# Kernel optimization log

Measured on AMD Instinct MI355X. Metric: run time of the kernel, lower is better.

Reference implementation:

```python
import math
import jax, jax.numpy as jnp
import numpy as np

B, N, DIN, DOUT = 64, 512, 256, 256
EPS = 1e-5  # torch BatchNorm1d default


def setup_inputs() -> dict:
    key = jax.random.key(0)
    k0, k1, k2, k3 = jax.random.split(key, 4)
    x = jax.random.normal(k0, (B, N, DIN), dtype=jnp.float32)
    # row-scaled dense adjacency (keeps activation magnitudes sane)
    adj = jax.random.uniform(k1, (B, N, N), dtype=jnp.float32) / N
    # prefix-style masks: first L_i nodes of each graph are valid
    lengths = jax.random.randint(k2, (B,), N // 4, N + 1)
    mask = (jnp.arange(N)[None, :] < lengths[:, None]).astype(jnp.float32)
    # xavier_normal_ init for weight
    std = math.sqrt(2.0 / (DIN + DOUT))
    weight = jax.random.normal(k3, (DIN, DOUT), dtype=jnp.float32) * std
    bias = jnp.zeros((DOUT,), dtype=jnp.float32)
    gamma = jnp.ones((DOUT,), dtype=jnp.float32)   # BN affine scale
    beta = jnp.zeros((DOUT,), dtype=jnp.float32)   # BN affine shift
    return {"x": x, "adj": adj, "mask": mask, "weight": weight,
            "bias": bias, "gamma": gamma, "beta": beta}


def reference(x, adj, mask, weight, bias, gamma, beta):
    # y = adj @ x @ W + b
    y = jnp.einsum('bnm,bmd->bnd', adj, x)
    y = jnp.einsum('bnd,de->bne', y, weight) + bias
    # masked BatchNorm1d (training mode): batch stats over all valid nodes,
    # equivalent to the torch code's pack -> BN -> unpack on prefix masks.
    m = mask[:, :, None]                       # [B, N, 1]
    n = jnp.sum(mask)                          # total valid nodes
    mean = jnp.sum(y * m, axis=(0, 1)) / n     # [DOUT]
    var = jnp.sum(((y - mean) ** 2) * m, axis=(0, 1)) / n  # biased var
    y = ((y - mean) * jax.lax.rsqrt(var + EPS) * gamma + beta) * m
    return jax.nn.relu(y)
```

## Files before the change

kernel.cpp:

```cpp
#include <hip/hip_runtime.h>

#define B_    64
#define N_    512
#define DIN_  256
#define DOUT_ 256
#define EPS_  1e-5f
#define ROWS_ (B_ * N_)
#define NBLK_Y2 512

typedef __attribute__((ext_vector_type(8))) short bf16x8;
typedef __attribute__((ext_vector_type(8))) unsigned short u16x8;
typedef __attribute__((ext_vector_type(4))) float f32x4;
typedef __attribute__((ext_vector_type(4))) short short4v;

__device__ __forceinline__ short f2bf(float f) {
    unsigned u = __builtin_bit_cast(unsigned, f);
    u += 0x7fff + ((u >> 16) & 1);
    return (short)(u >> 16);
}


__global__ __launch_bounds__(256) void wt_cvt(const float* __restrict__ W,
                                              short* __restrict__ WTf) {
    const int c = blockIdx.x * 256 + threadIdx.x;
    const int kf = c >> 10, ef = (c >> 6) & 15, lp = c & 63;
    const int e = ef * 16 + (lp & 15);
    const int k0 = kf * 32 + (lp >> 4) * 8;
    bf16x8 h;
    #pragma unroll
    for (int j = 0; j < 8; ++j)
        h[j] = f2bf(W[(size_t)(k0 + j) * DOUT_ + e]);
    *(bf16x8*)&WTf[(size_t)c * 8] = h;
}

__global__ __launch_bounds__(512, 4) void gemm_xw(const float* __restrict__ X,
                                                  const short* __restrict__ WTf,
                                                  short* __restrict__ xwT) {
    __shared__ __align__(16) short As[8 * 4 * 64 * 8];
    const int tid = threadIdx.x, wv = tid >> 6, lane = tid & 63;
    const int lrow = lane & 15, lg = lane >> 4;
    const int bid = blockIdx.x;
    const int rt = ((bid & 7) * 8 + ((bid >> 3) & 7)) * 8 + (bid >> 6);
    const int rowBase = rt * 64;

    #pragma unroll
    for (int j = 0; j < 4; ++j) {
        int s = tid + j * 512;
        int kf = s >> 8, mf = (s >> 6) & 3, lp = s & 63;
        int row = mf * 16 + (lp & 15);
        int k = kf * 32 + (lp >> 4) * 8;
        const float* src = &X[(size_t)(rowBase + row) * DIN_ + k];
        float4 v0 = *(const float4*)src;
        float4 v1 = *(const float4*)(src + 4);
        bf16x8 h = { f2bf(v0.x), f2bf(v0.y), f2bf(v0.z), f2bf(v0.w),
                     f2bf(v1.x), f2bf(v1.y), f2bf(v1.z), f2bf(v1.w) };
        *(bf16x8*)&As[s * 8] = h;
    }
    __syncthreads();

    const short* b0p = WTf + ((size_t)(wv * 2 + 0) * 64 + lane) * 8;
    const short* b1p = WTf + ((size_t)(wv * 2 + 1) * 64 + lane) * 8;
    bf16x8 bc0 = *(const bf16x8*)(b0p);
    bf16x8 bc1 = *(const bf16x8*)(b1p);
    f32x4 acc[4][2] = {};
    #pragma unroll 2
    for (int c = 0; c < 8; ++c) {
        const int cn = (c + 1 < 8) ? c + 1 : 7;
        bf16x8 bn0 = *(const bf16x8*)(b0p + cn * 8192);
        bf16x8 bn1 = *(const bf16x8*)(b1p + cn * 8192);
        const short* ab = &As[(c * 256 + lane) * 8];
        bf16x8 a0 = *(const bf16x8*)(ab);
        bf16x8 a1 = *(const bf16x8*)(ab + 512);
        bf16x8 a2 = *(const bf16x8*)(ab + 1024);
        bf16x8 a3 = *(const bf16x8*)(ab + 1536);
        acc[0][0] = __builtin_amdgcn_mfma_f32_16x16x32_bf16(a0, bc0, acc[0][0], 0, 0, 0);
        acc[0][1] = __builtin_amdgcn_mfma_f32_16x16x32_bf16(a0, bc1, acc[0][1], 0, 0, 0);
        acc[1][0] = __builtin_amdgcn_mfma_f32_16x16x32_bf16(a1, bc0, acc[1][0], 0, 0, 0);
        acc[1][1] = __builtin_amdgcn_mfma_f32_16x16x32_bf16(a1, bc1, acc[1][1], 0, 0, 0);
        acc[2][0] = __builtin_amdgcn_mfma_f32_16x16x32_bf16(a2, bc0, acc[2][0], 0, 0, 0);
        acc[2][1] = __builtin_amdgcn_mfma_f32_16x16x32_bf16(a2, bc1, acc[2][1], 0, 0, 0);
        acc[3][0] = __builtin_amdgcn_mfma_f32_16x16x32_bf16(a3, bc0, acc[3][0], 0, 0, 0);
        acc[3][1] = __builtin_amdgcn_mfma_f32_16x16x32_bf16(a3, bc1, acc[3][1], 0, 0, 0);
        bc0 = bn0; bc1 = bn1;
    }

    const int bz = rt >> 3, kfbase = (rt & 7) * 2;
    short* xwb = xwT + (size_t)bz * 131072;
    #pragma unroll
    for (int m = 0; m < 4; ++m)
        #pragma unroll
        for (int nf = 0; nf < 2; ++nf) {
            int kf = kfbase + (m >> 1);
            int ef = wv * 2 + nf;
            int lanep = lrow + 16 * ((m & 1) * 2 + (lg >> 1));
            size_t off = ((size_t)(kf * 16 + ef) * 64 + lanep) * 8 + (lg & 1) * 4;
            short4v o = { f2bf(acc[m][nf][0]), f2bf(acc[m][nf][1]),
                          f2bf(acc[m][nf][2]), f2bf(acc[m][nf][3]) };
            *(short4v*)&xwb[off] = o;
        }
}

template <bool BF16Y2>
__global__ __launch_bounds__(512, 4) void gemm_y2(const float* __restrict__ adj,
                                                  const short* __restrict__ xwT,
                                                  const float* __restrict__ bias,
                                                  const float* __restrict__ mask,
                                                  float* __restrict__ outf,
                                                  unsigned short* __restrict__ y2b,
                                                  float* __restrict__ psum,
                                                  float* __restrict__ psumsq,
                                                  float* __restrict__ pcnt) {
    __shared__ __align__(16) short As[16 * 4 * 64 * 8];
    const int tid = threadIdx.x, wv = tid >> 6, lane = tid & 63;
    const int lrow = lane & 15, lg = lane >> 4;
    const int bid = blockIdx.x;
    const int swz = ((bid & 7) << 6) | (bid >> 3);
    const int bz = swz >> 3, mt = swz & 7;
    const int rowBase = mt * 64;
    const float* A = adj + (size_t)bz * N_ * N_;
    const short* xwb = xwT + (size_t)bz * 131072;

    #pragma unroll
    for (int j = 0; j < 8; ++j) {
        int s = tid + j * 512;
        int kf = s >> 8, mf = (s >> 6) & 3, lp = s & 63;
        int row = mf * 16 + (lp & 15);
        int k = kf * 32 + (lp >> 4) * 8;
        const float* src = &A[(size_t)(rowBase + row) * N_ + k];
        float4 v0 = *(const float4*)src;
        float4 v1 = *(const float4*)(src + 4);
        bf16x8 h = { f2bf(v0.x), f2bf(v0.y), f2bf(v0.z), f2bf(v0.w),
                     f2bf(v1.x), f2bf(v1.y), f2bf(v1.z), f2bf(v1.w) };
        *(bf16x8*)&As[s * 8] = h;
    }
    __syncthreads();

    const short* b0p = xwb + ((size_t)(wv * 2 + 0) * 64 + lane) * 8;
    const short* b1p = xwb + ((size_t)(wv * 2 + 1) * 64 + lane) * 8;
    bf16x8 bpre[4][2];
    #pragma unroll
    for (int p = 0; p < 3; ++p) {
        bpre[p][0] = *(const bf16x8*)(b0p + p * 8192);
        bpre[p][1] = *(const bf16x8*)(b1p + p * 8192);
    }
    f32x4 acc[4][2] = {};
    #pragma unroll
    for (int c = 0; c < 16; ++c) {
        const int cn = (c + 3 < 16) ? c + 3 : 15;
        bpre[(c + 3) & 3][0] = *(const bf16x8*)(b0p + cn * 8192);
        bpre[(c + 3) & 3][1] = *(const bf16x8*)(b1p + cn * 8192);
        const short* ab = &As[(c * 256 + lane) * 8];
        bf16x8 a0 = *(const bf16x8*)(ab);
        bf16x8 a1 = *(const bf16x8*)(ab + 512);
        bf16x8 a2 = *(const bf16x8*)(ab + 1024);
        bf16x8 a3 = *(const bf16x8*)(ab + 1536);
        bf16x8 bc0 = bpre[c & 3][0];
        bf16x8 bc1 = bpre[c & 3][1];
        acc[0][0] = __builtin_amdgcn_mfma_f32_16x16x32_bf16(a0, bc0, acc[0][0], 0, 0, 0);
        acc[0][1] = __builtin_amdgcn_mfma_f32_16x16x32_bf16(a0, bc1, acc[0][1], 0, 0, 0);
        acc[1][0] = __builtin_amdgcn_mfma_f32_16x16x32_bf16(a1, bc0, acc[1][0], 0, 0, 0);
        acc[1][1] = __builtin_amdgcn_mfma_f32_16x16x32_bf16(a1, bc1, acc[1][1], 0, 0, 0);
        acc[2][0] = __builtin_amdgcn_mfma_f32_16x16x32_bf16(a2, bc0, acc[2][0], 0, 0, 0);
        acc[2][1] = __builtin_amdgcn_mfma_f32_16x16x32_bf16(a2, bc1, acc[2][1], 0, 0, 0);
        acc[3][0] = __builtin_amdgcn_mfma_f32_16x16x32_bf16(a3, bc0, acc[3][0], 0, 0, 0);
        acc[3][1] = __builtin_amdgcn_mfma_f32_16x16x32_bf16(a3, bc1, acc[3][1], 0, 0, 0);
    }

    float* C = outf + (size_t)bz * N_ * DOUT_;
    unsigned short* Cb = y2b + (size_t)bz * N_ * DOUT_;
    float mv[4][4];
    #pragma unroll
    for (int m = 0; m < 4; ++m)
        #pragma unroll
        for (int r = 0; r < 4; ++r)
            mv[m][r] = mask[bz * N_ + rowBase + m * 16 + lg * 4 + r];
    float sv[2] = {0.f, 0.f}, sq[2] = {0.f, 0.f};
    #pragma unroll
    for (int nf = 0; nf < 2; ++nf) {
        const int col = wv * 32 + nf * 16 + lrow;
        const float bv = bias[col];
        #pragma unroll
        for (int m = 0; m < 4; ++m) {
            const int r0 = rowBase + m * 16 + lg * 4;
            #pragma unroll
            for (int r = 0; r < 4; ++r) {
                float v = acc[m][nf][r] + bv;
                if (BF16Y2)
                    Cb[(size_t)(r0 + r) * DOUT_ + col] = (unsigned short)f2bf(v);
                else
                    C[(size_t)(r0 + r) * DOUT_ + col] = v;
                float vm = v * mv[m][r];
                sv[nf] += vm;
                sq[nf] = fmaf(v, vm, sq[nf]);
            }
        }
    }
    #pragma unroll
    for (int nf = 0; nf < 2; ++nf) {
        sv[nf] += __shfl_xor(sv[nf], 16); sv[nf] += __shfl_xor(sv[nf], 32);
        sq[nf] += __shfl_xor(sq[nf], 16); sq[nf] += __shfl_xor(sq[nf], 32);
    }
    const int pidx = bz * 8 + mt;
    if (lg == 0) {
        #pragma unroll
        for (int nf = 0; nf < 2; ++nf) {
            psum[(size_t)pidx * DOUT_ + wv * 32 + nf * 16 + lrow]   = sv[nf];
            psumsq[(size_t)pidx * DOUT_ + wv * 32 + nf * 16 + lrow] = sq[nf];
        }
    }
    if (wv == 0) {
        float cnt = mask[bz * N_ + rowBase + lane];
        #pragma unroll
        for (int i = 1; i < 64; i <<= 1) cnt += __shfl_xor(cnt, i);
        if (lane == 0) pcnt[pidx] = cnt;
    }
}

__global__ __launch_bounds__(256) void finalize2(const float* __restrict__ psum,
                                                 const float* __restrict__ psumsq,
                                                 const float* __restrict__ pcnt,
                                                 const float* __restrict__ gamma,
                                                 const float* __restrict__ beta,
                                                 float* __restrict__ scsh) {
    const int e = blockIdx.x, t = threadIdx.x;
    float s  = psum[(size_t)t * DOUT_ + e]   + psum[(size_t)(t + 256) * DOUT_ + e];
    float ss = psumsq[(size_t)t * DOUT_ + e] + psumsq[(size_t)(t + 256) * DOUT_ + e];
    float n  = pcnt[t] + pcnt[t + 256];
    #pragma unroll
    for (int i = 1; i < 64; i <<= 1) {
        s += __shfl_xor(s, i); ss += __shfl_xor(ss, i); n += __shfl_xor(n, i);
    }
    __shared__ float red[3][4];
    const int wv = t >> 6;
    if ((t & 63) == 0) { red[0][wv] = s; red[1][wv] = ss; red[2][wv] = n; }
    __syncthreads();
    if (t == 0) {
        s  = red[0][0] + red[0][1] + red[0][2] + red[0][3];
        ss = red[1][0] + red[1][1] + red[1][2] + red[1][3];
        n  = red[2][0] + red[2][1] + red[2][2] + red[2][3];
        float mean = s / n;
        float var = ss / n - mean * mean;
        float sc = rsqrtf(var + EPS_) * gamma[e];
        scsh[e] = sc;
        scsh[DOUT_ + e] = beta[e] - mean * sc;
    }
}

__global__ __launch_bounds__(256) void norm_relu_bf(const unsigned short* __restrict__ y2b,
                                                    const float* __restrict__ mask,
                                                    const float* __restrict__ scsh,
                                                    float* __restrict__ out) {
    const int nq = ROWS_ * (DOUT_ / 8);
    for (int q = blockIdx.x * blockDim.x + threadIdx.x; q < nq;
         q += gridDim.x * blockDim.x) {
        int e8 = (q & 31) * 8;
        int r = q >> 5;
        float m = mask[r];
        u16x8 uv = *(const u16x8*)&y2b[(size_t)q * 8];
        float4 sc0 = *(const float4*)&scsh[e8];
        float4 sc1 = *(const float4*)&scsh[e8 + 4];
        float4 sh0 = *(const float4*)&scsh[DOUT_ + e8];
        float4 sh1 = *(const float4*)&scsh[DOUT_ + e8 + 4];
        float4 o0, o1;
        #pragma unroll
        for (int j = 0; j < 4; ++j) {
            float f = __builtin_bit_cast(float, (unsigned)uv[j] << 16);
            (&o0.x)[j] = fmaxf(fmaf(f, (&sc0.x)[j], (&sh0.x)[j]) * m, 0.f);
        }
        #pragma unroll
        for (int j = 0; j < 4; ++j) {
            float f = __builtin_bit_cast(float, (unsigned)uv[j + 4] << 16);
            (&o1.x)[j] = fmaxf(fmaf(f, (&sc1.x)[j], (&sh1.x)[j]) * m, 0.f);
        }
        *(float4*)&out[(size_t)q * 8] = o0;
        *(float4*)&out[(size_t)q * 8 + 4] = o1;
    }
}

__global__ __launch_bounds__(256) void norm_relu_f32(float* __restrict__ y2,
                                                     const float* __restrict__ mask,
                                                     const float* __restrict__ scsh) {
    const int nq = ROWS_ * (DOUT_ / 4);
    for (int q = blockIdx.x * blockDim.x + threadIdx.x; q < nq;
         q += gridDim.x * blockDim.x) {
        int e4 = (q & 63) * 4;
        int r = q >> 6;
        float m = mask[r];
        float4 v  = *(float4*)&y2[(size_t)q * 4];
        float4 sc = *(const float4*)&scsh[e4];
        float4 sh = *(const float4*)&scsh[DOUT_ + e4];
        v.x = fmaxf(fmaf(v.x, sc.x, sh.x) * m, 0.f);
        v.y = fmaxf(fmaf(v.y, sc.y, sh.y) * m, 0.f);
        v.z = fmaxf(fmaf(v.z, sc.z, sh.z) * m, 0.f);
        v.w = fmaxf(fmaf(v.w, sc.w, sh.w) * m, 0.f);
        *(float4*)&y2[(size_t)q * 4] = v;
    }
}

extern "C" void kernel_launch(void* const* d_in, const int* in_sizes, int n_in,
                              void* d_out, int out_size, void* d_ws, size_t ws_size,
                              hipStream_t stream) {
    const float* x      = (const float*)d_in[0];
    const float* adj    = (const float*)d_in[1];
    const float* mask   = (const float*)d_in[2];
    const float* weight = (const float*)d_in[3];
    const float* bias   = (const float*)d_in[4];
    const float* gamma  = (const float*)d_in[5];
    const float* beta   = (const float*)d_in[6];
    float* out = (float*)d_out;

    const size_t xw_elems = (size_t)DOUT_ * ROWS_;
    const size_t need_bf = 131072 + xw_elems * 2 * 2 +
                           (size_t)NBLK_Y2 * DOUT_ * 4 * 2 + NBLK_Y2 * 4 + 2048 + 64;
    const bool use_bf = ws_size >= need_bf;

    short* WTf    = (short*)d_ws;
    short* xwT    = WTf + 256 * 256;
    unsigned short* y2b = (unsigned short*)(xwT + xw_elems);
    float* psum   = use_bf ? (float*)(y2b + xw_elems) : (float*)(y2b);
    float* psumsq = psum + NBLK_Y2 * DOUT_;
    float* pcnt   = psumsq + NBLK_Y2 * DOUT_;
    float* scsh   = pcnt + NBLK_Y2;

    wt_cvt<<<32, 256, 0, stream>>>(weight, WTf);
    gemm_xw<<<512, 512, 0, stream>>>(x, WTf, xwT);
    if (use_bf) {
        gemm_y2<true><<<NBLK_Y2, 512, 0, stream>>>(adj, xwT, bias, mask, out, y2b,
                                                   psum, psumsq, pcnt);
        finalize2<<<256, 256, 0, stream>>>(psum, psumsq, pcnt, gamma, beta, scsh);
        norm_relu_bf<<<2048, 256, 0, stream>>>(y2b, mask, scsh, out);
    } else {
        gemm_y2<false><<<NBLK_Y2, 512, 0, stream>>>(adj, xwT, bias, mask, out, y2b,
                                                    psum, psumsq, pcnt);
        finalize2<<<256, 256, 0, stream>>>(psum, psumsq, pcnt, gamma, beta, scsh);
        norm_relu_f32<<<2048, 256, 0, stream>>>(out, mask, scsh);
    }
}
```

Measured before the change: 55.52 us.

## Pre-convert adjacency to fragment-ordered bf16 and stream it directly in GEMM

```diff
diff --git a/kernel.cpp b/kernel.cpp
--- a/kernel.cpp
+++ b/kernel.cpp
@@ -31,6 +31,42 @@
     for (int j = 0; j < 8; ++j)
         h[j] = f2bf(W[(size_t)(k0 + j) * DOUT_ + e]);
     *(bf16x8*)&WTf[(size_t)c * 8] = h;
+}
+
+__global__ __launch_bounds__(512) void adj_cvt(const float* __restrict__ adj,
+                                               short* __restrict__ adjf) {
+    __shared__ short L[32 * 520];
+    const int tid = threadIdx.x;
+    const int bid = blockIdx.x;
+    const int swz = ((bid & 7) << 6) | (bid >> 3);
+    const int bz = swz >> 3, mt = swz & 7;
+    const float* A = adj + (size_t)bz * N_ * N_ + (size_t)mt * 64 * N_;
+    short* out = adjf + (size_t)(bz * 8 + mt) * 32768;
+
+    #pragma unroll
+    for (int h = 0; h < 2; ++h) {
+        if (h) __syncthreads();
+        const float* Ah = A + (size_t)h * 32 * N_;
+        #pragma unroll
+        for (int j = 0; j < 8; ++j) {
+            int o = j * 512 + tid;
+            int row = o >> 7, c4 = o & 127;
+            float4 v = *(const float4*)&Ah[(size_t)row * N_ + c4 * 4];
+            short4v s4 = { f2bf(v.x), f2bf(v.y), f2bf(v.z), f2bf(v.w) };
+            *(short4v*)&L[row * 520 + c4 * 4] = s4;
+        }
+        __syncthreads();
+        #pragma unroll
+        for (int j = 0; j < 4; ++j) {
+            int sh = j * 512 + tid;
+            int kf = sh >> 7, mfh = (sh >> 6) & 1, lp = sh & 63;
+            int rl = mfh * 16 + (lp & 15);
+            int k  = kf * 32 + (lp >> 4) * 8;
+            bf16x8 v = *(const bf16x8*)&L[rl * 520 + k];
+            int s = kf * 256 + (h * 2 + mfh) * 64 + lp;
+            *(bf16x8*)&out[(size_t)s * 8] = v;
+        }
+    }
 }
 
 __global__ __launch_bounds__(512, 4) void gemm_xw(const float* __restrict__ X,
@@ -101,15 +137,109 @@
 }
 
 template <bool BF16Y2>
-__global__ __launch_bounds__(512, 4) void gemm_y2(const float* __restrict__ adj,
-                                                  const short* __restrict__ xwT,
-                                                  const float* __restrict__ bias,
-                                                  const float* __restrict__ mask,
-                                                  float* __restrict__ outf,
-                                                  unsigned short* __restrict__ y2b,
-                                                  float* __restrict__ psum,
-                                                  float* __restrict__ psumsq,
-                                                  float* __restrict__ pcnt) {
+__global__ __launch_bounds__(512, 2) void gemm_y2f(const short* __restrict__ adjf,
+                                                   const short* __restrict__ xwT,
+                                                   const float* __restrict__ bias,
+                                                   const float* __restrict__ mask,
+                                                   float* __restrict__ outf,
+                                                   unsigned short* __restrict__ y2b,
+                                                   float* __restrict__ psum,
+                                                   float* __restrict__ psumsq,
+                                                   float* __restrict__ pcnt) {
+    const int tid = threadIdx.x, wv = tid >> 6, lane = tid & 63;
+    const int lrow = lane & 15, lg = lane >> 4;
+    const int bid = blockIdx.x;
+    const int swz = ((bid & 7) << 6) | (bid >> 3);
+    const int bz = swz >> 3, mt = swz & 7;
+    const int rowBase = mt * 64;
+    const short* ab  = adjf + (size_t)(bz * 8 + mt) * 32768;
+    const short* xwb = xwT + (size_t)bz * 131072;
+    const short* b0p = xwb + ((size_t)(wv * 2 + 0) * 64 + lane) * 8;
+    const short* b1p = xwb + ((size_t)(wv * 2 + 1) * 64 + lane) * 8;
+
+    bf16x8 aP[2][4], bP[2][2];
+    #pragma unroll
+    for (int m = 0; m < 4; ++m)
+        aP[0][m] = *(const bf16x8*)(ab + ((size_t)(0 * 4 + m) * 64 + lane) * 8);
+    bP[0][0] = *(const bf16x8*)(b0p);
+    bP[0][1] = *(const bf16x8*)(b1p);
+
+    f32x4 acc[4][2] = {};
+    #pragma unroll
+    for (int kf = 0; kf < 16; ++kf) {
+        const int cur = kf & 1, nxt = cur ^ 1;
+        if (kf < 15) {
+            #pragma unroll
+            for (int m = 0; m < 4; ++m)
+                aP[nxt][m] = *(const bf16x8*)(ab + ((size_t)((kf + 1) * 4 + m) * 64 + lane) * 8);
+            bP[nxt][0] = *(const bf16x8*)(b0p + (kf + 1) * 8192);
+            bP[nxt][1] = *(const bf16x8*)(b1p + (kf + 1) * 8192);
+        }
+        #pragma unroll
+        for (int m = 0; m < 4; ++m) {
+            acc[m][0] = __builtin_amdgcn_mfma_f32_16x16x32_bf16(aP[cur][m], bP[cur][0], acc[m][0], 0, 0, 0);
+            acc[m][1] = __builtin_amdgcn_mfma_f32_16x16x32_bf16(aP[cur][m], bP[cur][1], acc[m][1], 0, 0, 0);
+        }
+    }
+
+    float* C = outf + (size_t)bz * N_ * DOUT_;
+    unsigned short* Cb = y2b + (size_t)bz * N_ * DOUT_;
+    float mv[4][4];
+    #pragma unroll
+    for (int m = 0; m < 4; ++m)
+        #pragma unroll
+        for (int r = 0; r < 4; ++r)
+            mv[m][r] = mask[bz * N_ + rowBase + m * 16 + lg * 4 + r];
+    float sv[2] = {0.f, 0.f}, sq[2] = {0.f, 0.f};
+    #pragma unroll
+    for (int nf = 0; nf < 2; ++nf) {
+        const int col = wv * 32 + nf * 16 + lrow;
+        const float bv = bias[col];
+        #pragma unroll
+        for (int m = 0; m < 4; ++m) {
+            const int r0 = rowBase + m * 16 + lg * 4;
+            #pragma unroll
+            for (int r = 0; r < 4; ++r) {
+                float v = acc[m][nf][r] + bv;
+                if (BF16Y2)
+                    Cb[(size_t)(r0 + r) * DOUT_ + col] = (unsigned short)f2bf(v);
+                else
+                    C[(size_t)(r0 + r) * DOUT_ + col] = v;
+                float vm = v * mv[m][r];
+                sv[nf] += vm;
+                sq[nf] = fmaf(v, vm, sq[nf]);
+            }
+        }
+    }
+    #pragma unroll
+    for (int nf = 0; nf < 2; ++nf) {
+        sv[nf] += __shfl_xor(sv[nf], 16); sv[nf] += __shfl_xor(sv[nf], 32);
+        sq[nf] += __shfl_xor(sq[nf], 16); sq[nf] += __shfl_xor(sq[nf], 32);
+    }
+    const int pidx = bz * 8 + mt;
+    if (lg == 0) {
+        #pragma unroll
+        for (int nf = 0; nf < 2; ++nf) {
+            psum[(size_t)pidx * DOUT_ + wv * 32 + nf * 16 + lrow]   = sv[nf];
+            psumsq[(size_t)pidx * DOUT_ + wv * 32 + nf * 16 + lrow] = sq[nf];
+        }
+    }
+    if (wv == 0) {
+        float cnt = mask[bz * N_ + rowBase + lane];
+        #pragma unroll
+        for (int i = 1; i < 64; i <<= 1) cnt += __shfl_xor(cnt, i);
+        if (lane == 0) pcnt[pidx] = cnt;
+    }
+}
+
+__global__ __launch_bounds__(512, 4) void gemm_y2_stage(const float* __restrict__ adj,
+                                                        const short* __restrict__ xwT,
+                                                        const float* __restrict__ bias,
+                                                        const float* __restrict__ mask,
+                                                        unsigned short* __restrict__ y2b,
+                                                        float* __restrict__ psum,
+                                                        float* __restrict__ psumsq,
+                                                        float* __restrict__ pcnt) {
     __shared__ __align__(16) short As[16 * 4 * 64 * 8];
     const int tid = threadIdx.x, wv = tid >> 6, lane = tid & 63;
     const int lrow = lane & 15, lg = lane >> 4;
@@ -149,11 +279,11 @@
         const int cn = (c + 3 < 16) ? c + 3 : 15;
         bpre[(c + 3) & 3][0] = *(const bf16x8*)(b0p + cn * 8192);
         bpre[(c + 3) & 3][1] = *(const bf16x8*)(b1p + cn * 8192);
-        const short* ab = &As[(c * 256 + lane) * 8];
-        bf16x8 a0 = *(const bf16x8*)(ab);
-        bf16x8 a1 = *(const bf16x8*)(ab + 512);
-        bf16x8 a2 = *(const bf16x8*)(ab + 1024);
-        bf16x8 a3 = *(const bf16x8*)(ab + 1536);
+        const short* abp = &As[(c * 256 + lane) * 8];
+        bf16x8 a0 = *(const bf16x8*)(abp);
+        bf16x8 a1 = *(const bf16x8*)(abp + 512);
+        bf16x8 a2 = *(const bf16x8*)(abp + 1024);
+        bf16x8 a3 = *(const bf16x8*)(abp + 1536);
         bf16x8 bc0 = bpre[c & 3][0];
         bf16x8 bc1 = bpre[c & 3][1];
         acc[0][0] = __builtin_amdgcn_mfma_f32_16x16x32_bf16(a0, bc0, acc[0][0], 0, 0, 0);
@@ -166,7 +296,6 @@
         acc[3][1] = __builtin_amdgcn_mfma_f32_16x16x32_bf16(a3, bc1, acc[3][1], 0, 0, 0);
     }
 
-    float* C = outf + (size_t)bz * N_ * DOUT_;
     unsigned short* Cb = y2b + (size_t)bz * N_ * DOUT_;
     float mv[4][4];
     #pragma unroll
@@ -185,10 +314,7 @@
             #pragma unroll
             for (int r = 0; r < 4; ++r) {
                 float v = acc[m][nf][r] + bv;
-                if (BF16Y2)
-                    Cb[(size_t)(r0 + r) * DOUT_ + col] = (unsigned short)f2bf(v);
-                else
-                    C[(size_t)(r0 + r) * DOUT_ + col] = v;
+                Cb[(size_t)(r0 + r) * DOUT_ + col] = (unsigned short)f2bf(v);
                 float vm = v * mv[m][r];
                 sv[nf] += vm;
                 sq[nf] = fmaf(v, vm, sq[nf]);
@@ -309,30 +435,54 @@
     const float* beta   = (const float*)d_in[6];
     float* out = (float*)d_out;
 
-    const size_t xw_elems = (size_t)DOUT_ * ROWS_;
-    const size_t need_bf = 131072 + xw_elems * 2 * 2 +
-                           (size_t)NBLK_Y2 * DOUT_ * 4 * 2 + NBLK_Y2 * 4 + 2048 + 64;
-    const bool use_bf = ws_size >= need_bf;
-
-    short* WTf    = (short*)d_ws;
-    short* xwT    = WTf + 256 * 256;
-    unsigned short* y2b = (unsigned short*)(xwT + xw_elems);
-    float* psum   = use_bf ? (float*)(y2b + xw_elems) : (float*)(y2b);
-    float* psumsq = psum + NBLK_Y2 * DOUT_;
-    float* pcnt   = psumsq + NBLK_Y2 * DOUT_;
-    float* scsh   = pcnt + NBLK_Y2;
-
-    wt_cvt<<<32, 256, 0, stream>>>(weight, WTf);
-    gemm_xw<<<512, 512, 0, stream>>>(x, WTf, xwT);
-    if (use_bf) {
-        gemm_y2<true><<<NBLK_Y2, 512, 0, stream>>>(adj, xwT, bias, mask, out, y2b,
+    const size_t WTF_B   = 131072;
+    const size_t XWT_B   = (size_t)DOUT_ * ROWS_ * 2;
+    const size_t ADJF_B  = (size_t)B_ * 8 * 32768 * 2;
+    const size_t STATS_B = (size_t)NBLK_Y2 * DOUT_ * 4 * 2 + NBLK_Y2 * 4 + 2048;
+    const size_t Y2B_B   = (size_t)ROWS_ * DOUT_ * 2;
+
+    const bool has_adjf = ws_size >= WTF_B + XWT_B + ADJF_B + STATS_B;
+    const bool has_y2b_new = ws_size >= WTF_B + XWT_B + ADJF_B + STATS_B + Y2B_B;
+
+    char* p = (char*)d_ws;
+    short* WTf = (short*)p;                 p += WTF_B;
+    short* xwT = (short*)p;                 p += XWT_B;
+
+    if (has_adjf) {
+        short* adjf = (short*)p;            p += ADJF_B;
+        float* psum = (float*)p;
+        float* psumsq = psum + NBLK_Y2 * DOUT_;
+        float* pcnt = psumsq + NBLK_Y2 * DOUT_;
+        float* scsh = pcnt + NBLK_Y2;       p += STATS_B;
+        unsigned short* y2b = (unsigned short*)p;
+
+        wt_cvt<<<32, 256, 0, stream>>>(weight, WTf);
+        adj_cvt<<<512, 512, 0, stream>>>(adj, adjf);
+        gemm_xw<<<512, 512, 0, stream>>>(x, WTf, xwT);
+        if (has_y2b_new) {
+            gemm_y2f<true><<<NBLK_Y2, 512, 0, stream>>>(adjf, xwT, bias, mask, out,
+                                                        y2b, psum, psumsq, pcnt);
+            finalize2<<<256, 256, 0, stream>>>(psum, psumsq, pcnt, gamma, beta, scsh);
+            norm_relu_bf<<<2048, 256, 0, stream>>>(y2b, mask, scsh, out);
+        } else {
+            gemm_y2f<false><<<NBLK_Y2, 512, 0, stream>>>(adjf, xwT, bias, mask, out,
+                                                         (unsigned short*)out,
+                                                         psum, psumsq, pcnt);
+            finalize2<<<256, 256, 0, stream>>>(psum, psumsq, pcnt, gamma, beta, scsh);
+            norm_relu_f32<<<2048, 256, 0, stream>>>(out, mask, scsh);
+        }
+    } else {
+        unsigned short* y2b = (unsigned short*)p;  p += Y2B_B;
+        float* psum = (float*)p;
+        float* psumsq = psum + NBLK_Y2 * DOUT_;
+        float* pcnt = psumsq + NBLK_Y2 * DOUT_;
+        float* scsh = pcnt + NBLK_Y2;
+
+        wt_cvt<<<32, 256, 0, stream>>>(weight, WTf);
+        gemm_xw<<<512, 512, 0, stream>>>(x, WTf, xwT);
+        gemm_y2_stage<<<NBLK_Y2, 512, 0, stream>>>(adj, xwT, bias, mask, y2b,
                                                    psum, psumsq, pcnt);
         finalize2<<<256, 256, 0, stream>>>(psum, psumsq, pcnt, gamma, beta, scsh);
         norm_relu_bf<<<2048, 256, 0, stream>>>(y2b, mask, scsh, out);
-    } else {
-        gemm_y2<false><<<NBLK_Y2, 512, 0, stream>>>(adj, xwT, bias, mask, out, y2b,
-                                                    psum, psumsq, pcnt);
-        finalize2<<<256, 256, 0, stream>>>(psum, psumsq, pcnt, gamma, beta, scsh);
-        norm_relu_f32<<<2048, 256, 0, stream>>>(out, mask, scsh);
-    }
-}
+    }
+}
```

Measured after the change: 76.30 us. +37.4%, slower.
